# Performance work log

Hardware: AMD Instinct MI355X
Metric: run time of the kernel (lower is better)

Reference implementation:

```python
import jax, jax.numpy as jnp
import numpy as np


def setup_inputs() -> dict:
    key = jax.random.key(0)
    k1, k2, k3, k4 = jax.random.split(key, 4)
    N, IN, OUT, R, B = 8192, 256, 256, 8, 4
    a = jax.random.normal(k1, (N, N), dtype=jnp.float32)
    x = jax.random.normal(k2, (N, IN, R), dtype=jnp.float32)
    w_bases = jax.random.normal(k3, (B, IN, OUT), dtype=jnp.float32) * (1.0 / np.sqrt(IN))
    w_rel = jax.random.normal(k4, (R, B), dtype=jnp.float32) * 0.5
    return {"a": a, "x": x, "w_bases": w_bases, "w_rel": w_rel}


def reference(a, x, w_bases, w_rel):
    # Basis-combined per-relation weights: [R, IN, OUT]
    w = jnp.einsum('rb,bio->rio', w_rel, w_bases)
    # Per-relation aggregation: support_r = a @ x[:, :, r] -> stack as [N, R, IN]
    # (matches torch.cat([a @ x[:,:,r] for r], dim=1) ordering)
    supports = jnp.einsum('nm,mir->nri', a, x)  # [N, R, IN]
    # tmp [N, R*IN] @ weights [R*IN, OUT] fused as one einsum
    out = jnp.einsum('nri,rio->no', supports, w)  # [N, OUT]
    return out
```

## Files before the change

### kernel.cpp

```cpp
#include <hip/hip_runtime.h>
#include <hip/hip_bf16.h>
#include <stdint.h>

typedef __fp16 f16x2 __attribute__((ext_vector_type(2)));
typedef __fp16 f16x8 __attribute__((ext_vector_type(8)));
typedef float  f32x4 __attribute__((ext_vector_type(4)));

#define GLOBAL_AS __attribute__((address_space(1)))
#define LDS_AS    __attribute__((address_space(3)))

#define NN   8192
#define INC  256
#define OUTC 256
#define K2   2048
#define YTN  ((size_t)OUTC * NN)

__device__ __forceinline__ void async_copy16(const void* g, void* l) {
    __builtin_amdgcn_global_load_lds((const GLOBAL_AS uint32_t*)g,
                                     (LDS_AS uint32_t*)l, 16, 0, 0);
}

__global__ void build_w2t16(const float* __restrict__ wb, const float* __restrict__ wr,
                            __fp16* __restrict__ W2T16) {
    int o = blockIdx.x;
    int i = threadIdx.x;
    float s[8];
#pragma unroll
    for (int r = 0; r < 8; ++r) s[r] = 0.f;
#pragma unroll
    for (int b = 0; b < 4; ++b) {
        float w = wb[((size_t)((b << 8) + i)) * OUTC + o];
#pragma unroll
        for (int r = 0; r < 8; ++r) s[r] = fmaf(wr[r * 4 + b], w, s[r]);
    }
    f16x8 out;
    f16x2* p = (f16x2*)&out;
    p[0] = __builtin_amdgcn_cvt_pkrtz(s[0], s[1]);
    p[1] = __builtin_amdgcn_cvt_pkrtz(s[2], s[3]);
    p[2] = __builtin_amdgcn_cvt_pkrtz(s[4], s[5]);
    p[3] = __builtin_amdgcn_cvt_pkrtz(s[6], s[7]);
    *reinterpret_cast<f16x8*>(&W2T16[(size_t)o * K2 + i * 8]) = out;
}

constexpr int BM = 128, BN = 128, BK = 32;

template <bool AF32, bool BF32>
__global__ __launch_bounds__(256, 2)
void gemm_mixed(const void* __restrict__ Ap, const void* __restrict__ Bp,
                float* __restrict__ Cp, int M, int N, int K, int kPerSplit) {
    constexpr int ABYTES = BM * BK * (AF32 ? 4 : 2);
    constexpr int BBYTES = BN * BK * (BF32 ? 4 : 2);
    __shared__ __align__(16) char smem[ABYTES + BBYTES];
    char* As = smem;
    char* Bs = smem + ABYTES;

    const int bm = blockIdx.x * BM;
    const int bn = blockIdx.y * BN;
    const int k0 = blockIdx.z * kPerSplit;

    const int tid  = threadIdx.x;
    const int lane = tid & 63;
    const int wave = tid >> 6;
    const int wm   = (wave >> 1) * 64;
    const int wn   = (wave & 1) * 64;
    const int quad = lane >> 4;
    const int l16  = lane & 15;

    f32x4 acc[4][4];
#pragma unroll
    for (int ti = 0; ti < 4; ++ti)
#pragma unroll
        for (int tj = 0; tj < 4; ++tj)
            acc[ti][tj] = (f32x4){0.f, 0.f, 0.f, 0.f};

    for (int kc = k0; kc < k0 + kPerSplit; kc += BK) {
        if (AF32) {
            const float* Ag = (const float*)Ap;
#pragma unroll
            for (int i = 0; i < 4; ++i) {
                int r0 = wave * 32 + i * 8;
                const float* g = Ag + (size_t)(bm + r0 + (lane >> 3)) * K + kc + ((lane & 7) << 2);
                async_copy16(g, As + (size_t)r0 * BK * 4);
            }
        } else {
            const __fp16* Ag = (const __fp16*)Ap;
#pragma unroll
            for (int i = 0; i < 2; ++i) {
                int r0 = wave * 32 + i * 16;
                const __fp16* g = Ag + (size_t)(bm + r0 + (lane >> 2)) * K + kc + ((lane & 3) << 3);
                async_copy16(g, As + (size_t)r0 * BK * 2);
            }
        }
        if (BF32) {
            const float* Bg = (const float*)Bp;
#pragma unroll
            for (int i = 0; i < 4; ++i) {
                int r0 = wave * 32 + i * 8;
                const float* g = Bg + (size_t)(bn + r0 + (lane >> 3)) * K + kc + ((lane & 7) << 2);
                async_copy16(g, Bs + (size_t)r0 * BK * 4);
            }
        } else {
            const __fp16* Bg = (const __fp16*)Bp;
#pragma unroll
            for (int i = 0; i < 2; ++i) {
                int r0 = wave * 32 + i * 16;
                const __fp16* g = Bg + (size_t)(bn + r0 + (lane >> 2)) * K + kc + ((lane & 3) << 3);
                async_copy16(g, Bs + (size_t)r0 * BK * 2);
            }
        }
        __syncthreads();

        f16x8 af[4], bf[4];
#pragma unroll
        for (int t = 0; t < 4; ++t) {
            if (AF32) {
                const float* Ar = (const float*)As + (size_t)(wm + t * 16 + l16) * BK + quad * 8;
                f32x4 u0 = *(const f32x4*)Ar;
                f32x4 u1 = *(const f32x4*)(Ar + 4);
                f16x2* p = (f16x2*)&af[t];
                p[0] = __builtin_amdgcn_cvt_pkrtz(u0[0], u0[1]);
                p[1] = __builtin_amdgcn_cvt_pkrtz(u0[2], u0[3]);
                p[2] = __builtin_amdgcn_cvt_pkrtz(u1[0], u1[1]);
                p[3] = __builtin_amdgcn_cvt_pkrtz(u1[2], u1[3]);
            } else {
                af[t] = *(const f16x8*)((const __fp16*)As + (size_t)(wm + t * 16 + l16) * BK + quad * 8);
            }
            if (BF32) {
                const float* Br = (const float*)Bs + (size_t)(wn + t * 16 + l16) * BK + quad * 8;
                f32x4 u0 = *(const f32x4*)Br;
                f32x4 u1 = *(const f32x4*)(Br + 4);
                f16x2* p = (f16x2*)&bf[t];
                p[0] = __builtin_amdgcn_cvt_pkrtz(u0[0], u0[1]);
                p[1] = __builtin_amdgcn_cvt_pkrtz(u0[2], u0[3]);
                p[2] = __builtin_amdgcn_cvt_pkrtz(u1[0], u1[1]);
                p[3] = __builtin_amdgcn_cvt_pkrtz(u1[2], u1[3]);
            } else {
                bf[t] = *(const f16x8*)((const __fp16*)Bs + (size_t)(wn + t * 16 + l16) * BK + quad * 8);
            }
        }
#pragma unroll
        for (int ti = 0; ti < 4; ++ti)
#pragma unroll
            for (int tj = 0; tj < 4; ++tj)
                acc[ti][tj] = __builtin_amdgcn_mfma_f32_16x16x32_f16(
                    af[ti], bf[tj], acc[ti][tj], 0, 0, 0);
        __syncthreads();
    }

    float* Cz = Cp + (size_t)blockIdx.z * M * N;
#pragma unroll
    for (int ti = 0; ti < 4; ++ti)
#pragma unroll
        for (int tj = 0; tj < 4; ++tj)
#pragma unroll
            for (int r = 0; r < 4; ++r) {
                int row = bm + wm + ti * 16 + quad * 4 + r;
                int col = bn + wn + tj * 16 + l16;
                Cz[(size_t)row * N + col] = acc[ti][tj][r];
            }
}

__global__ void reduce_yT(const float* __restrict__ yTp, __fp16* __restrict__ yT16) {
    size_t base = ((size_t)blockIdx.x * 256 + threadIdx.x) * 8;
    f32x4 s0 = (f32x4){0.f, 0.f, 0.f, 0.f};
    f32x4 s1 = (f32x4){0.f, 0.f, 0.f, 0.f};
#pragma unroll
    for (int z = 0; z < 4; ++z) {
        const float* p = yTp + (size_t)z * YTN + base;
        s0 += *(const f32x4*)p;
        s1 += *(const f32x4*)(p + 4);
    }
    f16x8 out;
    f16x2* p = (f16x2*)&out;
    p[0] = __builtin_amdgcn_cvt_pkrtz(s0[0], s0[1]);
    p[1] = __builtin_amdgcn_cvt_pkrtz(s0[2], s0[3]);
    p[2] = __builtin_amdgcn_cvt_pkrtz(s1[0], s1[1]);
    p[3] = __builtin_amdgcn_cvt_pkrtz(s1[2], s1[3]);
    *reinterpret_cast<f16x8*>(&yT16[base]) = out;
}

__global__ void reduce_out(const float* __restrict__ op, float* __restrict__ out) {
    size_t base = ((size_t)blockIdx.x * 256 + threadIdx.x) * 4;
    f32x4 s = (f32x4){0.f, 0.f, 0.f, 0.f};
#pragma unroll
    for (int z = 0; z < 8; ++z)
        s += *(const f32x4*)(op + (size_t)z * YTN + base);
    *reinterpret_cast<f32x4*>(&out[base]) = s;
}

extern "C" void kernel_launch(void* const* d_in, const int* in_sizes, int n_in,
                              void* d_out, int out_size, void* d_ws, size_t ws_size,
                              hipStream_t stream) {
    const float* a  = (const float*)d_in[0];
    const float* x  = (const float*)d_in[1];
    const float* wb = (const float*)d_in[2];
    const float* wr = (const float*)d_in[3];
    float* out = (float*)d_out;

    char* w = (char*)d_ws;
    float*  yT_p  = (float*)(w);
    __fp16* yT16  = (__fp16*)(w + ((size_t)32 << 20));
    float*  out_p = (float*)(w + ((size_t)36 << 20));
    __fp16* W2T16 = (__fp16*)(w + ((size_t)100 << 20));

    build_w2t16<<<dim3(256), dim3(256), 0, stream>>>(wb, wr, W2T16);

    gemm_mixed<false, true><<<dim3(2, 64, 4), dim3(256), 0, stream>>>(
        W2T16, x, yT_p, 256, NN, K2, 512);

    reduce_yT<<<dim3(1024), dim3(256), 0, stream>>>(yT_p, yT16);

    gemm_mixed<true, false><<<dim3(64, 2, 8), dim3(256), 0, stream>>>(
        a, yT16, out_p, NN, OUTC, NN, 1024);

    reduce_out<<<dim3(2048), dim3(256), 0, stream>>>(out_p, out);
}
```

Before: 499.9 us.

## Use full-width 128x256 tile for second GEMM to read A once

Adds a dedicated kernel for the a @ yT GEMM whose block tile covers all 256 output columns, replacing the two column blocks per row tile. Each fp32 element of the large adjacency matrix is then loaded and converted to fp16 once instead of twice, halving A traffic and conversion work. The cost is doubled accumulator registers per wave and half as many blocks, which may reduce occupancy and latency hiding.

```diff
diff --git a/kernel.cpp b/kernel.cpp
--- a/kernel.cpp
+++ b/kernel.cpp
@@ -160,6 +160,86 @@
             }
 }
 
+constexpr int BM2 = 128, BN2 = 256, BK2 = 32;
+
+__global__ __launch_bounds__(256, 2)
+void gemm2_wide(const float* __restrict__ Ap, const __fp16* __restrict__ Bp,
+                float* __restrict__ Cp, int M, int K, int kPerSplit) {
+    __shared__ __align__(16) char smem[BM2 * BK2 * 4 + BN2 * BK2 * 2];
+    char* As = smem;
+    char* Bs = smem + BM2 * BK2 * 4;
+
+    const int bm = blockIdx.x * BM2;
+    const int k0 = blockIdx.z * kPerSplit;
+
+    const int tid  = threadIdx.x;
+    const int lane = tid & 63;
+    const int wave = tid >> 6;
+    const int wm   = (wave >> 1) * 64;
+    const int wn   = (wave & 1) * 128;
+    const int quad = lane >> 4;
+    const int l16  = lane & 15;
+
+    f32x4 acc[4][8];
+#pragma unroll
+    for (int ti = 0; ti < 4; ++ti)
+#pragma unroll
+        for (int tj = 0; tj < 8; ++tj)
+            acc[ti][tj] = (f32x4){0.f, 0.f, 0.f, 0.f};
+
+    for (int kc = k0; kc < k0 + kPerSplit; kc += BK2) {
+#pragma unroll
+        for (int i = 0; i < 4; ++i) {
+            int r0 = wave * 32 + i * 8;
+            const float* g = Ap + (size_t)(bm + r0 + (lane >> 3)) * K + kc + ((lane & 7) << 2);
+            async_copy16(g, As + (size_t)r0 * BK2 * 4);
+        }
+#pragma unroll
+        for (int i = 0; i < 4; ++i) {
+            int r0 = wave * 64 + i * 16;
+            const __fp16* g = Bp + (size_t)(r0 + (lane >> 2)) * K + kc + ((lane & 3) << 3);
+            async_copy16(g, Bs + (size_t)r0 * BK2 * 2);
+        }
+        __syncthreads();
+
+        f16x8 af[4], bf[8];
+#pragma unroll
+        for (int t = 0; t < 4; ++t) {
+            const float* Ar = (const float*)As + (size_t)(wm + t * 16 + l16) * BK2 + quad * 8;
+            f32x4 u0 = *(const f32x4*)Ar;
+            f32x4 u1 = *(const f32x4*)(Ar + 4);
+            f16x2* p = (f16x2*)&af[t];
+            p[0] = __builtin_amdgcn_cvt_pkrtz(u0[0], u0[1]);
+            p[1] = __builtin_amdgcn_cvt_pkrtz(u0[2], u0[3]);
+            p[2] = __builtin_amdgcn_cvt_pkrtz(u1[0], u1[1]);
+            p[3] = __builtin_amdgcn_cvt_pkrtz(u1[2], u1[3]);
+        }
+#pragma unroll
+        for (int t = 0; t < 8; ++t)
+            bf[t] = *(const f16x8*)((const __fp16*)Bs + (size_t)(wn + t * 16 + l16) * BK2 + quad * 8);
+
+#pragma unroll
+        for (int ti = 0; ti < 4; ++ti)
+#pragma unroll
+            for (int tj = 0; tj < 8; ++tj)
+                acc[ti][tj] = __builtin_amdgcn_mfma_f32_16x16x32_f16(
+                    af[ti], bf[tj], acc[ti][tj], 0, 0, 0);
+        __syncthreads();
+    }
+
+    float* Cz = Cp + (size_t)blockIdx.z * M * BN2;
+#pragma unroll
+    for (int ti = 0; ti < 4; ++ti)
+#pragma unroll
+        for (int tj = 0; tj < 8; ++tj)
+#pragma unroll
+            for (int r = 0; r < 4; ++r) {
+                int row = bm + wm + ti * 16 + quad * 4 + r;
+                int col = wn + tj * 16 + l16;
+                Cz[(size_t)row * BN2 + col] = acc[ti][tj][r];
+            }
+}
+
 __global__ void reduce_yT(const float* __restrict__ yTp, __fp16* __restrict__ yT16) {
     size_t base = ((size_t)blockIdx.x * 256 + threadIdx.x) * 8;
     f32x4 s0 = (f32x4){0.f, 0.f, 0.f, 0.f};
@@ -210,8 +290,8 @@
 
     reduce_yT<<<dim3(1024), dim3(256), 0, stream>>>(yT_p, yT16);
 
-    gemm_mixed<true, false><<<dim3(64, 2, 8), dim3(256), 0, stream>>>(
-        a, yT16, out_p, NN, OUTC, NN, 1024);
+    gemm2_wide<<<dim3(64, 1, 8), dim3(256), 0, stream>>>(
+        a, yT16, out_p, NN, NN, 1024);
 
     reduce_out<<<dim3(2048), dim3(256), 0, stream>>>(out_p, out);
 }
```

Result: faster. 470.0 us (-6.0%).
